# Kernel tuning notes

Hardware: AMD Instinct MI355X
Metric: run time of the kernel (lower is better)

Reference implementation:

```python
import jax, jax.numpy as jnp
import numpy as np

DIM = 512
NUM_HEADS = 8
HEAD_DIM = DIM // NUM_HEADS
KERNEL = (3, 5, 5)  # (kd, kh, kw), must be odd and <= spatial dims
B, D, H, W = 1, 6, 48, 96


def setup_inputs() -> dict:
    key = jax.random.key(0)
    ks = jax.random.split(key, 5)
    x = jax.random.normal(ks[0], (B, D, H, W, DIM), jnp.float32)
    w_qkv = jax.random.normal(ks[1], (DIM, 3 * DIM), jnp.float32) * 0.02
    b_qkv = jax.random.normal(ks[2], (3 * DIM,), jnp.float32) * 0.02
    w_proj = jax.random.normal(ks[3], (DIM, DIM), jnp.float32) * 0.02
    b_proj = jax.random.normal(ks[4], (DIM,), jnp.float32) * 0.02
    return {"x": x, "w_qkv": w_qkv, "b_qkv": b_qkv, "w_proj": w_proj, "b_proj": b_proj}


def _nbhd_idx(L, k):
    # NATTEN neighborhood: window of exactly k keys, centered, shifted inward at edges.
    p = jnp.arange(L)
    start = jnp.clip(p - k // 2, 0, L - k)
    return start[:, None] + jnp.arange(k)[None, :]  # [L, k]


def _na3d(q, k, v, kernel):
    # q, k, v: [B, D, H, W, heads, hd]; q pre-scaled.
    kd, kh, kw = kernel
    _, Dd, Hh, Ww, _, _ = q.shape
    idx_d = _nbhd_idx(Dd, kd)
    idx_h = _nbhd_idx(Hh, kh)
    idx_w = _nbhd_idx(Ww, kw)
    offs = jnp.stack(
        jnp.meshgrid(jnp.arange(kd), jnp.arange(kh), jnp.arange(kw), indexing="ij"),
        axis=-1,
    ).reshape(-1, 3)  # [K3, 3]

    def shift(t, o):
        # gather the o-th neighbor of every query position along each spatial axis
        t = jnp.take(t, jnp.take(idx_d, o[0], axis=1), axis=1)
        t = jnp.take(t, jnp.take(idx_h, o[1], axis=1), axis=2)
        t = jnp.take(t, jnp.take(idx_w, o[2], axis=1), axis=3)
        return t

    def score_step(_, o):
        k_s = shift(k, o)
        s = jnp.einsum("bdhwnc,bdhwnc->bdhwn", q, k_s)
        return None, s

    _, scores = jax.lax.scan(score_step, None, offs)  # [K3, B, D, H, W, heads]
    attn = jax.nn.softmax(scores, axis=0)

    def out_step(acc, xs):
        o, a = xs
        v_s = shift(v, o)
        return acc + a[..., None] * v_s, None

    out, _ = jax.lax.scan(out_step, jnp.zeros_like(q), (offs, attn))
    return out


def reference(x, w_qkv, b_qkv, w_proj, b_proj):
    Bb, Dd, Hh, Ww, C = x.shape
    qkv = (x @ w_qkv + b_qkv).reshape(Bb, Dd, Hh, Ww, 3, NUM_HEADS, HEAD_DIM)
    q = qkv[..., 0, :, :]
    k = qkv[..., 1, :, :]
    v = qkv[..., 2, :, :]
    scale = HEAD_DIM ** (-0.5)
    # Faithful to source: module scales q by self.scale, then tuned_na3d applies
    # head_dim**-0.5 again inside the fused kernel -> net q * head_dim**-1.
    q = q * (scale * scale)
    out = _na3d(q, k, v, KERNEL).reshape(Bb, Dd, Hh, Ww, C)
    return out @ w_proj + b_proj
```

## Files before the change

kernel.cpp:

```cpp
#include <hip/hip_runtime.h>

#define DIMC   512
#define NHEADS 8
#define HDIM   64
#define DD     6
#define HHH    48
#define WWW    96
#define NPOS   (DD * HHH * WWW)

typedef unsigned short u16;
typedef __attribute__((ext_vector_type(8))) short bf16x8;
typedef __attribute__((ext_vector_type(4))) float f32x4;

static __device__ __forceinline__ float b2f(u16 u) {
    return __builtin_bit_cast(float, (unsigned)u << 16);
}
static __device__ __forceinline__ u16 f2b(float f) {
    unsigned x = __builtin_bit_cast(unsigned, f);
    return (u16)((x + 0x7fffu + ((x >> 16) & 1u)) >> 16);
}

static __device__ __forceinline__ void gload_lds16(const void* g, void* l) {
    __builtin_amdgcn_global_load_lds((const __attribute__((address_space(1))) void*)g,
                                     (__attribute__((address_space(3))) void*)l, 16, 0, 0);
}

__global__ __launch_bounds__(256) void cvt_x_bf16(const float* __restrict__ in,
                                                  u16* __restrict__ out, int n4) {
    const int i = blockIdx.x * 256 + threadIdx.x;
    float4 v = reinterpret_cast<const float4*>(in)[i];
    ushort4 o = { f2b(v.x), f2b(v.y), f2b(v.z), f2b(v.w) };
    reinterpret_cast<ushort4*>(out)[i] = o;
}

__global__ __launch_bounds__(256) void cvt_wqkvT(const float* __restrict__ w,
                                                 u16* __restrict__ o) {
    const int id = blockIdx.x * 256 + threadIdx.x;
    const int nn = id >> 9, kk = id & 511;
    o[id] = f2b(w[(size_t)kk * 1536 + nn]);
}

__global__ __launch_bounds__(256) void cvt_wprojT(const float* __restrict__ w,
                                                  u16* __restrict__ o) {
    const int id = blockIdx.x * 256 + threadIdx.x;
    const int nn = id >> 9, kk = id & 511;
    o[id] = f2b(w[(size_t)kk * 512 + nn]);
}

__global__ __launch_bounds__(256) void gemm_bf16_mfma(
    const u16* __restrict__ A, int lda,
    const u16* __restrict__ B, int ldb,
    const float* __restrict__ bias, int Kp,
    void* __restrict__ Cout, int ldc, int cmode, int nx)
{
    __shared__ u16 As[128 * 64];
    __shared__ u16 Bs[128 * 64];

    const int tid = threadIdx.x;
    const int l   = tid & 63;
    const int w   = tid >> 6;
    const int wr  = w >> 1, wc = w & 1;

    const int cpx = gridDim.x >> 3;
    const int idp = (blockIdx.x & 7) * cpx + (blockIdx.x >> 3);
    const int by  = idp / nx;
    const int bx  = idp - by * nx;
    const int m0  = by * 128;
    const int n0  = bx * 128;

    const int srow = tid >> 3;
    const int schk = ((tid & 7) ^ (srow & 7)) * 8;

    const u16* ga = A + (size_t)(m0 + srow) * lda + schk;
    const u16* gb = B + (size_t)(n0 + srow) * ldb + schk;
    const size_t a32 = (size_t)32 * lda;
    const size_t b32 = (size_t)32 * ldb;
    u16* const la0 = As + (w * 8) * 64;
    u16* const lb0 = Bs + (w * 8) * 64;

    f32x4 acc[4][4];
#pragma unroll
    for (int i = 0; i < 4; i++)
#pragma unroll
        for (int j = 0; j < 4; j++) acc[i][j] = (f32x4)0.0f;

    const int c   = l & 15;
    const int g   = l >> 4;
    const int lk0 = (((0 * 4 + g) ^ (c & 7))) * 8;
    const int lk1 = (((1 * 4 + g) ^ (c & 7))) * 8;

#pragma unroll 1
    for (int k0 = 0; k0 < Kp; k0 += 64) {
#pragma unroll
        for (int q = 0; q < 4; ++q) {
            gload_lds16(ga + q * a32, la0 + q * 32 * 64);
            gload_lds16(gb + q * b32, lb0 + q * 32 * 64);
        }
        ga += 64; gb += 64;
        __syncthreads();

        {
            bf16x8 af[4], bfr[4];
#pragma unroll
            for (int f = 0; f < 4; f++) {
                af[f]  = *reinterpret_cast<const bf16x8*>(&As[(wr * 64 + f * 16 + c) * 64 + lk0]);
                bfr[f] = *reinterpret_cast<const bf16x8*>(&Bs[(wc * 64 + f * 16 + c) * 64 + lk0]);
            }
#pragma unroll
            for (int i = 0; i < 4; i++)
#pragma unroll
                for (int j = 0; j < 4; j++)
                    acc[i][j] = __builtin_amdgcn_mfma_f32_16x16x32_bf16(af[i], bfr[j], acc[i][j], 0, 0, 0);
        }
        {
            bf16x8 af[4], bfr[4];
#pragma unroll
            for (int f = 0; f < 4; f++) {
                af[f]  = *reinterpret_cast<const bf16x8*>(&As[(wr * 64 + f * 16 + c) * 64 + lk1]);
                bfr[f] = *reinterpret_cast<const bf16x8*>(&Bs[(wc * 64 + f * 16 + c) * 64 + lk1]);
            }
#pragma unroll
            for (int i = 0; i < 4; i++)
#pragma unroll
                for (int j = 0; j < 4; j++)
                    acc[i][j] = __builtin_amdgcn_mfma_f32_16x16x32_bf16(af[i], bfr[j], acc[i][j], 0, 0, 0);
        }
        __syncthreads();
    }

#pragma unroll
    for (int i = 0; i < 4; i++) {
        const int mb = m0 + wr * 64 + i * 16 + g * 4;
#pragma unroll
        for (int j = 0; j < 4; j++) {
            const int n = n0 + wc * 64 + j * 16 + c;
            const float bv = bias[n];
#pragma unroll
            for (int r = 0; r < 4; r++) {
                const float v = acc[i][j][r] + bv;
                if (cmode) reinterpret_cast<u16*>(Cout)[(size_t)(mb + r) * ldc + n] = f2b(v);
                else       reinterpret_cast<float*>(Cout)[(size_t)(mb + r) * ldc + n] = v;
            }
        }
    }
}

__global__ __launch_bounds__(512, 4) void na3d_mfma(
    const u16* __restrict__ qkv, u16* __restrict__ attnc)
{
    __shared__ int   rowoff[192];
    __shared__ int   dlt[16];
    __shared__ u16   Vt[NHEADS][64][36];
    __shared__ float ssum_lds[NHEADS][16];

    const int bid  = blockIdx.x;
    const int tile = (bid & 7) * 216 + (bid >> 3);
    const int pd  = tile / 288;
    const int rem = tile - pd * 288;
    const int h0  = (rem / 24) * 4;
    const int w0  = (rem % 24) * 4;
    const int sd  = min(max(pd - 1, 0), DD - 3);
    const int shb = min(max(h0 - 2, 0), HHH - 5);
    const int swb = min(max(w0 - 2, 0), WWW - 5);

    const int tid = threadIdx.x;
    if (tid < 192) {
        const int dd = tid >> 6, hh = (tid >> 3) & 7, wu = tid & 7;
        const int row = (sd + dd) * (HHH * WWW)
                      + min(shb + hh, HHH - 1) * WWW + min(swb + wu, WWW - 1);
        rowoff[tid] = row * 1536;
    }
    if (tid < 16) {
        const int ph = h0 + (tid >> 2), pw = w0 + (tid & 3);
        const int dh = min(max(ph - 2, 0), HHH - 5) - shb;
        const int dw = min(max(pw - 2, 0), WWW - 5) - swb;
        dlt[tid] = (dh << 4) | dw;
    }
    __syncthreads();

    const int head = tid >> 6;
    const int l    = tid & 63;
    const int g    = l >> 4;
    const int c    = l & 15;

    const int qrowi = pd * (HHH * WWW) + (h0 + (c >> 2)) * WWW + (w0 + (c & 3));
    const u16* qrow = qkv + (size_t)qrowi * 1536 + head * HDIM;
    const bf16x8 qlo = *reinterpret_cast<const bf16x8*>(qrow + 8 * g);
    const bf16x8 qhi = *reinterpret_cast<const bf16x8*>(qrow + 32 + 8 * g);
    const int dparts = dlt[c];
    const int dh = dparts >> 4, dw = dparts & 15;

    f32x4 oacc[4];
#pragma unroll
    for (int j = 0; j < 4; j++) oacc[j] = (f32x4)0.0f;
    float ssum = 0.0f;

    const float SC = 0.022542110f;

#pragma unroll 1
    for (int s = 0; s < 6; ++s) {
        {
            const int npair = l >> 2;
            const int chq   = l & 3;
#pragma unroll
            for (int rr = 0; rr < 2; ++rr) {
                const int ch8 = 8 * chq + 32 * rr;
                const int2 rp = *reinterpret_cast<const int2*>(&rowoff[s * 32 + 2 * npair]);
                const ushort4* pa = reinterpret_cast<const ushort4*>(qkv + rp.x + 1024 + head * HDIM + ch8);
                const ushort4* pb = reinterpret_cast<const ushort4*>(qkv + rp.y + 1024 + head * HDIM + ch8);
                ushort4 va0 = pa[0], va1 = pa[1];
                ushort4 vb0 = pb[0], vb1 = pb[1];
                const u16* va = reinterpret_cast<const u16*>(&va0);
                const u16* vb = reinterpret_cast<const u16*>(&vb0);
#pragma unroll
                for (int e = 0; e < 4; ++e) {
                    unsigned dwo = (unsigned)va[e] | ((unsigned)vb[e] << 16);
                    *reinterpret_cast<unsigned*>(&Vt[head][ch8 + e][2 * npair]) = dwo;
                }
                const u16* va2 = reinterpret_cast<const u16*>(&va1);
                const u16* vb2 = reinterpret_cast<const u16*>(&vb1);
#pragma unroll
                for (int e = 0; e < 4; ++e) {
                    unsigned dwo = (unsigned)va2[e] | ((unsigned)vb2[e] << 16);
                    *reinterpret_cast<unsigned*>(&Vt[head][ch8 + 4 + e][2 * npair]) = dwo;
                }
            }
        }

        unsigned pA, pB, pC, pD;
#pragma unroll
        for (int t = 0; t < 2; ++t) {
            const int sb0 = s * 32 + t * 16;
            const int ro  = rowoff[sb0 + c];
            const u16* kr = qkv + ro + 512 + head * HDIM;
            const bf16x8 klo = *reinterpret_cast<const bf16x8*>(kr + 8 * g);
            const bf16x8 khi = *reinterpret_cast<const bf16x8*>(kr + 32 + 8 * g);
            f32x4 sf = (f32x4)0.0f;
            sf = __builtin_amdgcn_mfma_f32_16x16x32_bf16(klo, qlo, sf, 0, 0, 0);
            sf = __builtin_amdgcn_mfma_f32_16x16x32_bf16(khi, qhi, sf, 0, 0, 0);
            const int sb  = sb0 + 4 * g;
            const int wu0 = sb & 7;
            const int hh_ = (sb >> 3) & 7;
            const bool hv = ((unsigned)(hh_ - dh) < 5u);
            float e0, e1, e2, e3;
            e0 = (hv && (unsigned)(wu0 + 0 - dw) < 5u) ? exp2f(sf[0] * SC) : 0.0f;
            e1 = (hv && (unsigned)(wu0 + 1 - dw) < 5u) ? exp2f(sf[1] * SC) : 0.0f;
            e2 = (hv && (unsigned)(wu0 + 2 - dw) < 5u) ? exp2f(sf[2] * SC) : 0.0f;
            e3 = (hv && (unsigned)(wu0 + 3 - dw) < 5u) ? exp2f(sf[3] * SC) : 0.0f;
            ssum += e0 + e1 + e2 + e3;
            const unsigned p01 = (unsigned)f2b(e0) | ((unsigned)f2b(e1) << 16);
            const unsigned p23 = (unsigned)f2b(e2) | ((unsigned)f2b(e3) << 16);
            if (t == 0) { pA = p01; pB = p23; }
            else        { pC = p01; pD = p23; }
        }

        asm volatile("v_permlane32_swap_b32 %0, %1" : "+v"(pA), "+v"(pC));
        asm volatile("v_permlane32_swap_b32 %0, %1" : "+v"(pB), "+v"(pD));
        asm volatile("v_permlane16_swap_b32 %0, %1" : "+v"(pA), "+v"(pC));
        asm volatile("v_permlane16_swap_b32 %0, %1" : "+v"(pB), "+v"(pD));

        {
            const int4 pv = make_int4((int)pA, (int)pB, (int)pC, (int)pD);
            const bf16x8 pfrag = __builtin_bit_cast(bf16x8, pv);
#pragma unroll
            for (int j = 0; j < 4; ++j) {
                const uint2 v01 = *reinterpret_cast<const uint2*>(&Vt[head][16 * j + c][8 * g]);
                const uint2 v23 = *reinterpret_cast<const uint2*>(&Vt[head][16 * j + c][8 * g + 4]);
                const int4 vv = make_int4((int)v01.x, (int)v01.y, (int)v23.x, (int)v23.y);
                const bf16x8 vfrag = __builtin_bit_cast(bf16x8, vv);
                oacc[j] = __builtin_amdgcn_mfma_f32_16x16x32_bf16(pfrag, vfrag, oacc[j], 0, 0, 0);
            }
        }
    }

    ssum += __shfl_xor(ssum, 16);
    ssum += __shfl_xor(ssum, 32);
    if (l < 16) ssum_lds[head][c] = ssum;
    const f32x4 sums4 = *reinterpret_cast<const f32x4*>(&ssum_lds[head][4 * g]);

    const int orow = pd * (HHH * WWW) + (h0 + g) * WWW + w0;
#pragma unroll
    for (int r = 0; r < 4; ++r) {
        const float inv = 1.0f / sums4[r];
        u16* base = attnc + (size_t)(orow + r) * 512 + head * HDIM;
#pragma unroll
        for (int j = 0; j < 4; ++j)
            base[16 * j + c] = f2b(oacc[j][r] * inv);
    }
}

extern "C" void kernel_launch(void* const* d_in, const int* in_sizes, int n_in,
                              void* d_out, int out_size, void* d_ws, size_t ws_size,
                              hipStream_t stream)
{
    const float* x      = (const float*)d_in[0];
    const float* w_qkv  = (const float*)d_in[1];
    const float* b_qkv  = (const float*)d_in[2];
    const float* w_proj = (const float*)d_in[3];
    const float* b_proj = (const float*)d_in[4];
    float* out = (float*)d_out;

    u16* qkvb   = (u16*)d_ws;
    u16* attnc  = qkvb  + (size_t)NPOS * 1536;
    u16* xb     = attnc + (size_t)NPOS * 512;
    u16* wqkvT  = xb    + (size_t)NPOS * 512;
    u16* wprojT = wqkvT + (size_t)1536 * 512;

    cvt_x_bf16<<<(NPOS * 512 / 4) / 256, 256, 0, stream>>>(x, xb, NPOS * 512 / 4);
    cvt_wqkvT<<<(1536 * 512) / 256, 256, 0, stream>>>(w_qkv, wqkvT);
    cvt_wprojT<<<(512 * 512) / 256, 256, 0, stream>>>(w_proj, wprojT);

    gemm_bf16_mfma<<<(1536 / 128) * (NPOS / 128), 256, 0, stream>>>(
        xb, 512, wqkvT, 512, b_qkv, 512, qkvb, 1536, 1, 1536 / 128);

    na3d_mfma<<<NPOS / 16, 512, 0, stream>>>(qkvb, attnc);

    gemm_bf16_mfma<<<(512 / 128) * (NPOS / 128), 256, 0, stream>>>(
        attnc, 512, wprojT, 512, b_proj, 512, out, 512, 0, 512 / 128);
}
```

Baseline: 180.0 us.

## Merge conversion kernels and enlarge GEMM tile to 256x128 with 8 waves

Folds the three fp32-to-bf16 conversion kernels into one launch that splits work by block index. The GEMM block grows from 256 to 512 threads and from a 128x128 to a 256x128 output tile, with new global-to-LDS load addressing. The goal is to cut launch overhead and raise B-tile reuse per block. The larger block and shared-memory footprint may lower occupancy, and the wave-to-tile mapping outside the visible hunks must match the new 8-wave layout.

```diff
diff --git a/kernel.cpp b/kernel.cpp
--- a/kernel.cpp
+++ b/kernel.cpp
@@ -25,58 +25,62 @@
                                      (__attribute__((address_space(3))) void*)l, 16, 0, 0);
 }
 
-__global__ __launch_bounds__(256) void cvt_x_bf16(const float* __restrict__ in,
-                                                  u16* __restrict__ out, int n4) {
-    const int i = blockIdx.x * 256 + threadIdx.x;
-    float4 v = reinterpret_cast<const float4*>(in)[i];
-    ushort4 o = { f2b(v.x), f2b(v.y), f2b(v.z), f2b(v.w) };
-    reinterpret_cast<ushort4*>(out)[i] = o;
-}
-
-__global__ __launch_bounds__(256) void cvt_wqkvT(const float* __restrict__ w,
-                                                 u16* __restrict__ o) {
-    const int id = blockIdx.x * 256 + threadIdx.x;
-    const int nn = id >> 9, kk = id & 511;
-    o[id] = f2b(w[(size_t)kk * 1536 + nn]);
-}
-
-__global__ __launch_bounds__(256) void cvt_wprojT(const float* __restrict__ w,
-                                                  u16* __restrict__ o) {
-    const int id = blockIdx.x * 256 + threadIdx.x;
-    const int nn = id >> 9, kk = id & 511;
-    o[id] = f2b(w[(size_t)kk * 512 + nn]);
-}
-
-__global__ __launch_bounds__(256) void gemm_bf16_mfma(
+__global__ __launch_bounds__(256) void cvt_all(
+    const float* __restrict__ x, const float* __restrict__ w_qkv,
+    const float* __restrict__ w_proj, u16* __restrict__ xb,
+    u16* __restrict__ wqkvT, u16* __restrict__ wprojT)
+{
+    const int bid = blockIdx.x;
+    const int tid = threadIdx.x;
+    if (bid < 13824) {
+        const int i = bid * 256 + tid;
+        float4 v = reinterpret_cast<const float4*>(x)[i];
+        ushort4 o = { f2b(v.x), f2b(v.y), f2b(v.z), f2b(v.w) };
+        reinterpret_cast<ushort4*>(xb)[i] = o;
+    } else if (bid < 13824 + 3072) {
+        const int id = (bid - 13824) * 256 + tid;
+        const int nn = id >> 9, kk = id & 511;
+        wqkvT[id] = f2b(w_qkv[(size_t)kk * 1536 + nn]);
+    } else {
+        const int id = (bid - 16896) * 256 + tid;
+        const int nn = id >> 9, kk = id & 511;
+        wprojT[id] = f2b(w_proj[(size_t)kk * 512 + nn]);
+    }
+}
+
+__global__ __launch_bounds__(512) void gemm_bf16_mfma(
     const u16* __restrict__ A, int lda,
     const u16* __restrict__ B, int ldb,
     const float* __restrict__ bias, int Kp,
     void* __restrict__ Cout, int ldc, int cmode, int nx)
 {
-    __shared__ u16 As[128 * 64];
+    __shared__ u16 As[256 * 64];
     __shared__ u16 Bs[128 * 64];
 
     const int tid = threadIdx.x;
     const int l   = tid & 63;
     const int w   = tid >> 6;
-    const int wr  = w >> 1, wc = w & 1;
+    const int wr  = w >> 1;
+    const int wc  = w & 1;
 
     const int cpx = gridDim.x >> 3;
     const int idp = (blockIdx.x & 7) * cpx + (blockIdx.x >> 3);
     const int by  = idp / nx;
     const int bx  = idp - by * nx;
-    const int m0  = by * 128;
+    const int m0  = by * 256;
     const int n0  = bx * 128;
 
-    const int srow = tid >> 3;
-    const int schk = ((tid & 7) ^ (srow & 7)) * 8;
-
-    const u16* ga = A + (size_t)(m0 + srow) * lda + schk;
-    const u16* gb = B + (size_t)(n0 + srow) * ldb + schk;
-    const size_t a32 = (size_t)32 * lda;
-    const size_t b32 = (size_t)32 * ldb;
-    u16* const la0 = As + (w * 8) * 64;
-    u16* const lb0 = Bs + (w * 8) * 64;
+    const int lrow = l >> 3;
+    const int swz  = ((l & 7) ^ lrow) * 8;
+    const int arow = w * 32 + lrow;
+    const int brow = w * 16 + lrow;
+
+    const u16* ga = A + (size_t)(m0 + arow) * lda + swz;
+    const u16* gb = B + (size_t)(n0 + brow) * ldb + swz;
+    const size_t a8 = (size_t)8 * lda;
+    const size_t b8 = (size_t)8 * ldb;
+    u16* const la0 = As + w * 2048;
+    u16* const lb0 = Bs + w * 1024;
 
     f32x4 acc[4][4];
 #pragma unroll
@@ -86,16 +90,17 @@
 
     const int c   = l & 15;
     const int g   = l >> 4;
-    const int lk0 = (((0 * 4 + g) ^ (c & 7))) * 8;
-    const int lk1 = (((1 * 4 + g) ^ (c & 7))) * 8;
+    const int lk0 = ((0 * 4 + g) ^ (c & 7)) * 8;
+    const int lk1 = ((1 * 4 + g) ^ (c & 7)) * 8;
 
 #pragma unroll 1
     for (int k0 = 0; k0 < Kp; k0 += 64) {
 #pragma unroll
-        for (int q = 0; q < 4; ++q) {
-            gload_lds16(ga + q * a32, la0 + q * 32 * 64);
-            gload_lds16(gb + q * b32, lb0 + q * 32 * 64);
-        }
+        for (int q = 0; q < 4; ++q)
+            gload_lds16(ga + q * a8, la0 + q * 512);
+#pragma unroll
+        for (int q = 0; q < 2; ++q)
+            gload_lds16(gb + q * b8, lb0 + q * 512);
         ga += 64; gb += 64;
         __syncthreads();
 
@@ -306,15 +311,13 @@
     u16* wqkvT  = xb    + (size_t)NPOS * 512;
     u16* wprojT = wqkvT + (size_t)1536 * 512;
 
-    cvt_x_bf16<<<(NPOS * 512 / 4) / 256, 256, 0, stream>>>(x, xb, NPOS * 512 / 4);
-    cvt_wqkvT<<<(1536 * 512) / 256, 256, 0, stream>>>(w_qkv, wqkvT);
-    cvt_wprojT<<<(512 * 512) / 256, 256, 0, stream>>>(w_proj, wprojT);
-
-    gemm_bf16_mfma<<<(1536 / 128) * (NPOS / 128), 256, 0, stream>>>(
+    cvt_all<<<17920, 256, 0, stream>>>(x, w_qkv, w_proj, xb, wqkvT, wprojT);
+
+    gemm_bf16_mfma<<<(NPOS / 256) * (1536 / 128), 512, 0, stream>>>(
         xb, 512, wqkvT, 512, b_qkv, 512, qkvb, 1536, 1, 1536 / 128);
 
     na3d_mfma<<<NPOS / 16, 512, 0, stream>>>(qkvb, attnc);
 
-    gemm_bf16_mfma<<<(512 / 128) * (NPOS / 128), 256, 0, stream>>>(
+    gemm_bf16_mfma<<<(NPOS / 256) * (512 / 128), 512, 0, stream>>>(
         attnc, 512, wprojT, 512, b_proj, 512, out, 512, 0, 512 / 128);
 }
```

After: 162.8 us. 9.6% less time.
